# Kernel tuning notes

Measured on AMD Instinct MI355X. Metric: run time of the kernel, lower is better.

The kernel has to match this reference:

```python
import jax, jax.numpy as jnp
import numpy as np

PI = 3.1415926  # matches the truncated pi used in the torch source
BS = 8          # DCT block size (qmat.shape[1:] == (8, 8))
NQ = 16         # number of learned quant matrices (qmat.shape[0])
IMG = 64        # nn.Fold output_size=(64, 64)


def dct_matrix(n):
    # Reproduces the (slightly nonstandard) basis built in DCT2d.__init__.
    C = np.zeros((n, n), dtype=np.float32)
    C[0, :] = np.sqrt(1.0 / n)
    for i in range(1, n):
        for j in range(n):
            C[i, j] = np.cos(PI * i * (2 * j + 1) / (2.0 * n)) * np.sqrt(2.0 / n)
    return jnp.asarray(C)


def setup_inputs() -> dict:
    key = jax.random.key(0)
    ks = jax.random.split(key, 9)
    B, Ch = 32, 256
    x = jax.random.normal(ks[0], (B, Ch, IMG, IMG), dtype=jnp.float32)
    noise_level = jax.random.uniform(ks[1], (1,), dtype=jnp.float32)
    # learned parameters
    qmat = jax.random.uniform(ks[2], (NQ, BS, BS), dtype=jnp.float32)
    qmat_weights = jnp.ones((NQ,), dtype=jnp.float32)
    # noise_level_net: Linear(1,16) -> GELU -> Linear(16,16) -> GELU -> Linear(16, 2+NQ)
    w1 = jax.random.normal(ks[3], (1, 16), dtype=jnp.float32) * 0.5
    b1 = jnp.zeros((16,), dtype=jnp.float32)
    w2 = jax.random.normal(ks[4], (16, 16), dtype=jnp.float32) * 0.25
    b2 = jnp.zeros((16,), dtype=jnp.float32)
    w3 = jax.random.normal(ks[5], (16, 2 + NQ), dtype=jnp.float32) * 0.25
    b3 = jnp.zeros((2 + NQ,), dtype=jnp.float32)
    return {"x": x, "noise_level": noise_level, "qmat": qmat,
            "qmat_weights": qmat_weights, "w1": w1, "b1": b1,
            "w2": w2, "b2": b2, "w3": w3, "b3": b3}


def reference(x, noise_level, qmat, qmat_weights, w1, b1, w2, b2, w3, b3):
    B, Ch, H, W = x.shape
    Cm = dct_matrix(BS)
    Cmt = Cm.T

    # noise_level_net (torch.nn.GELU default = exact erf)
    h = jax.nn.gelu(noise_level @ w1 + b1, approximate=False)
    h = jax.nn.gelu(h @ w2 + b2, approximate=False)
    nr = h @ w3 + b3  # [2 + NQ]

    qw = jax.nn.softmax(qmat_weights) * nr[0] + nr[1]          # [NQ]
    learned_qmat = jnp.einsum('i,ihw->hw', qw * nr[2:], qmat)  # [8, 8]

    # unfold into non-overlapping 8x8 blocks: [B*Ch, L, 8, 8], L = (H/8)*(W/8)
    blocks = x.reshape(B * Ch, H // BS, BS, W // BS, BS)
    blocks = blocks.transpose(0, 1, 3, 2, 4).reshape(B * Ch, -1, BS, BS)

    # 2D DCT per block: C @ X @ C^T
    blocks_dct = jnp.einsum('ij,nljk,km->nlim', Cm, blocks, Cmt)
    # IDCT of mask-weighted spectra: C^T @ X @ C
    low = jnp.einsum('ij,nljk,km->nlim', Cmt, blocks_dct * learned_qmat, Cm)
    high = jnp.einsum('ij,nljk,km->nlim', Cmt, blocks_dct * (1.0 - learned_qmat), Cm)

    def fold(b):  # inverse of the unfold above
        b = b.reshape(B * Ch, H // BS, W // BS, BS, BS)
        return b.transpose(0, 1, 3, 2, 4).reshape(B, Ch, H, W)

    return fold(low), fold(high)
```

## Files before the change

kernel.cpp:

```cpp
#include <hip/hip_runtime.h>
#include <math.h>


typedef float f4 __attribute__((ext_vector_type(4)));

__host__ __device__ constexpr float cc(int i, int j) {
  constexpr double COS16[32] = {
     1.0,
     0.98078528040323043,
     0.92387953251128674,
     0.83146961230254524,
     0.70710678118654752,
     0.55557023301960222,
     0.38268343236508977,
     0.19509032201612827,
     0.0,
    -0.19509032201612827,
    -0.38268343236508977,
    -0.55557023301960222,
    -0.70710678118654752,
    -0.83146961230254524,
    -0.92387953251128674,
    -0.98078528040323043,
    -1.0,
    -0.98078528040323043,
    -0.92387953251128674,
    -0.83146961230254524,
    -0.70710678118654752,
    -0.55557023301960222,
    -0.38268343236508977,
    -0.19509032201612827,
     0.0,
     0.19509032201612827,
     0.38268343236508977,
     0.55557023301960222,
     0.70710678118654752,
     0.83146961230254524,
     0.92387953251128674,
     0.98078528040323043,
  };
  return (i == 0) ? 0.35355339059327373f
                  : (float)(0.5 * COS16[(i * (2 * j + 1)) % 32]);
}

__global__ void setup_q(const float* __restrict__ noise,
                        const float* __restrict__ qmat,
                        const float* __restrict__ qmw,
                        const float* __restrict__ w1, const float* __restrict__ b1,
                        const float* __restrict__ w2, const float* __restrict__ b2,
                        const float* __restrict__ w3, const float* __restrict__ b3,
                        float* __restrict__ qout) {
  __shared__ double coeff[16];
  if (threadIdx.x == 0) {
    const double inv_sqrt2 = 0.70710678118654752;
    double h1[16], h2[16], nr[18];
    double nl = (double)noise[0];
    for (int j = 0; j < 16; ++j) {
      double v = nl * (double)w1[j] + (double)b1[j];
      h1[j] = 0.5 * v * (1.0 + erf(v * inv_sqrt2));
    }
    for (int j = 0; j < 16; ++j) {
      double v = (double)b2[j];
      for (int i = 0; i < 16; ++i) v += h1[i] * (double)w2[i * 16 + j];
      h2[j] = 0.5 * v * (1.0 + erf(v * inv_sqrt2));
    }
    for (int j = 0; j < 18; ++j) {
      double v = (double)b3[j];
      for (int i = 0; i < 16; ++i) v += h2[i] * (double)w3[i * 18 + j];
      nr[j] = v;
    }
    double mx = (double)qmw[0];
    for (int i = 1; i < 16; ++i) mx = fmax(mx, (double)qmw[i]);
    double e[16], s = 0.0;
    for (int i = 0; i < 16; ++i) { e[i] = exp((double)qmw[i] - mx); s += e[i]; }
    for (int i = 0; i < 16; ++i)
      coeff[i] = (e[i] / s * nr[0] + nr[1]) * nr[2 + i];
  }
  __syncthreads();
  const int t = threadIdx.x;
  double q = 0.0;
  for (int i = 0; i < 16; ++i) q += coeff[i] * (double)qmat[i * 64 + t];
  qout[t] = (float)q;
}

__global__ __launch_bounds__(256) void dct_main(const float* __restrict__ x,
                                                const float* __restrict__ qg,
                                                float* __restrict__ lo,
                                                float* __restrict__ hi) {
  __shared__ float Qs[64];
  const int tid = threadIdx.x;
  if (tid < 64) Qs[tid] = qg[tid];
  __syncthreads();

  const int gid = blockIdx.x * 256 + tid;
  const int base = ((gid >> 6) << 12) | (((gid >> 3) & 7) << 9) | ((gid & 7) << 3);
  const float* px = x + base;

  float X[8][8];
#pragma unroll
  for (int r = 0; r < 8; ++r) {
    const f4 a = __builtin_nontemporal_load(reinterpret_cast<const f4*>(px + r * 64));
    const f4 b = __builtin_nontemporal_load(reinterpret_cast<const f4*>(px + r * 64 + 4));
    X[r][0] = a.x; X[r][1] = a.y; X[r][2] = a.z; X[r][3] = a.w;
    X[r][4] = b.x; X[r][5] = b.y; X[r][6] = b.z; X[r][7] = b.w;
  }

  float U[8][8];
#pragma unroll
  for (int r = 0; r < 8; ++r) {
#pragma unroll
    for (int j = 0; j < 8; ++j) {
      float s = X[r][0] * cc(j, 0);
#pragma unroll
      for (int l = 1; l < 8; ++l) s = fmaf(X[r][l], cc(j, l), s);
      U[r][j] = s;
    }
  }
#pragma unroll
  for (int j = 0; j < 8; ++j) {
    float t[8];
#pragma unroll
    for (int i = 0; i < 8; ++i) {
      float s = cc(i, 0) * U[0][j];
#pragma unroll
      for (int k = 1; k < 8; ++k) s = fmaf(cc(i, k), U[k][j], s);
      t[i] = s;
    }
#pragma unroll
    for (int i = 0; i < 8; ++i) U[i][j] = t[i] * Qs[i * 8 + j];
  }
#pragma unroll
  for (int r = 0; r < 8; ++r) {
    float t[8];
#pragma unroll
    for (int j = 0; j < 8; ++j) {
      float s = U[r][0] * cc(0, j);
#pragma unroll
      for (int k = 1; k < 8; ++k) s = fmaf(U[r][k], cc(k, j), s);
      t[j] = s;
    }
#pragma unroll
    for (int j = 0; j < 8; ++j) U[r][j] = t[j];
  }
#pragma unroll
  for (int j = 0; j < 8; ++j) {
    float t[8];
#pragma unroll
    for (int i = 0; i < 8; ++i) {
      float s = cc(0, i) * U[0][j];
#pragma unroll
      for (int k = 1; k < 8; ++k) s = fmaf(cc(k, i), U[k][j], s);
      t[i] = s;
    }
#pragma unroll
    for (int i = 0; i < 8; ++i) U[i][j] = t[i];
  }

  float* plo = lo + base;
  float* phi = hi + base;
#pragma unroll
  for (int r = 0; r < 8; ++r) {
    f4 a = {U[r][0], U[r][1], U[r][2], U[r][3]};
    f4 b = {U[r][4], U[r][5], U[r][6], U[r][7]};
    *reinterpret_cast<f4*>(plo + r * 64)     = a;
    *reinterpret_cast<f4*>(plo + r * 64 + 4) = b;
    f4 c = {X[r][0] - U[r][0], X[r][1] - U[r][1],
            X[r][2] - U[r][2], X[r][3] - U[r][3]};
    f4 d = {X[r][4] - U[r][4], X[r][5] - U[r][5],
            X[r][6] - U[r][6], X[r][7] - U[r][7]};
    *reinterpret_cast<f4*>(phi + r * 64)     = c;
    *reinterpret_cast<f4*>(phi + r * 64 + 4) = d;
  }
}

extern "C" void kernel_launch(void* const* d_in, const int* in_sizes, int n_in,
                              void* d_out, int out_size, void* d_ws, size_t ws_size,
                              hipStream_t stream) {
  const float* x   = (const float*)d_in[0];
  const float* nl  = (const float*)d_in[1];
  const float* qm  = (const float*)d_in[2];
  const float* qmw = (const float*)d_in[3];
  const float* w1  = (const float*)d_in[4];
  const float* b1  = (const float*)d_in[5];
  const float* w2  = (const float*)d_in[6];
  const float* b2  = (const float*)d_in[7];
  const float* w3  = (const float*)d_in[8];
  const float* b3  = (const float*)d_in[9];

  const int n_elem = in_sizes[0];
  float* lo = (float*)d_out;
  float* hi = lo + n_elem;
  float* q  = (float*)d_ws;

  setup_q<<<1, 64, 0, stream>>>(nl, qm, qmw, w1, b1, w2, b2, w3, b3, q);

  const int n_blocks8 = n_elem >> 6;
  const int grid = n_blocks8 >> 8;
  dct_main<<<grid, 256, 0, stream>>>(x, q, lo, hi);
}
```

Baseline: 429.9 us.

## Split each 8x8 DCT block across 8 lanes with shuffle transposes

Instead of one thread holding a whole 8x8 block in registers, each wave now processes 8 blocks with every lane holding one row, and transposes between passes with three xor-shuffle stages. This cuts per-thread register pressure, raising occupancy (launch bounds now request 8 blocks per SM). Each lane's row load is now strided, but lanes in a wave cover contiguous 512-element bands for better coalescing. The trade-off is extra cross-lane shuffle instructions.

```diff
diff --git a/kernel.cpp b/kernel.cpp
--- a/kernel.cpp
+++ b/kernel.cpp
@@ -83,93 +83,95 @@
   qout[t] = (float)q;
 }
 
-__global__ __launch_bounds__(256) void dct_main(const float* __restrict__ x,
-                                                const float* __restrict__ qg,
-                                                float* __restrict__ lo,
-                                                float* __restrict__ hi) {
+__device__ __forceinline__ void transpose8(float v[8], int r) {
+#pragma unroll
+  for (int k = 0; k < 3; ++k) {
+    const int bit = 1 << k;
+    const int lm = 8 << k;
+    const bool rb = (r >> k) & 1;
+#pragma unroll
+    for (int j0 = 0; j0 < 8; ++j0) {
+      if (j0 & bit) continue;
+      const int j1 = j0 | bit;
+      float s = rb ? v[j0] : v[j1];
+      float t = __shfl_xor(s, lm, 64);
+      v[j0] = rb ? t : v[j0];
+      v[j1] = rb ? v[j1] : t;
+    }
+  }
+}
+
+__global__ __launch_bounds__(256, 8) void dct_main(const float* __restrict__ x,
+                                                   const float* __restrict__ qg,
+                                                   float* __restrict__ lo,
+                                                   float* __restrict__ hi) {
   __shared__ float Qs[64];
   const int tid = threadIdx.x;
   if (tid < 64) Qs[tid] = qg[tid];
   __syncthreads();
 
-  const int gid = blockIdx.x * 256 + tid;
-  const int base = ((gid >> 6) << 12) | (((gid >> 3) & 7) << 9) | ((gid & 7) << 3);
-  const float* px = x + base;
-
-  float X[8][8];
-#pragma unroll
-  for (int r = 0; r < 8; ++r) {
-    const f4 a = __builtin_nontemporal_load(reinterpret_cast<const f4*>(px + r * 64));
-    const f4 b = __builtin_nontemporal_load(reinterpret_cast<const f4*>(px + r * 64 + 4));
-    X[r][0] = a.x; X[r][1] = a.y; X[r][2] = a.z; X[r][3] = a.w;
-    X[r][4] = b.x; X[r][5] = b.y; X[r][6] = b.z; X[r][7] = b.w;
-  }
-
-  float U[8][8];
-#pragma unroll
-  for (int r = 0; r < 8; ++r) {
-#pragma unroll
-    for (int j = 0; j < 8; ++j) {
-      float s = X[r][0] * cc(j, 0);
-#pragma unroll
-      for (int l = 1; l < 8; ++l) s = fmaf(X[r][l], cc(j, l), s);
-      U[r][j] = s;
-    }
-  }
-#pragma unroll
-  for (int j = 0; j < 8; ++j) {
-    float t[8];
-#pragma unroll
-    for (int i = 0; i < 8; ++i) {
-      float s = cc(i, 0) * U[0][j];
-#pragma unroll
-      for (int k = 1; k < 8; ++k) s = fmaf(cc(i, k), U[k][j], s);
-      t[i] = s;
-    }
-#pragma unroll
-    for (int i = 0; i < 8; ++i) U[i][j] = t[i] * Qs[i * 8 + j];
-  }
-#pragma unroll
-  for (int r = 0; r < 8; ++r) {
-    float t[8];
-#pragma unroll
-    for (int j = 0; j < 8; ++j) {
-      float s = U[r][0] * cc(0, j);
-#pragma unroll
-      for (int k = 1; k < 8; ++k) s = fmaf(U[r][k], cc(k, j), s);
-      t[j] = s;
-    }
-#pragma unroll
-    for (int j = 0; j < 8; ++j) U[r][j] = t[j];
-  }
-#pragma unroll
-  for (int j = 0; j < 8; ++j) {
-    float t[8];
-#pragma unroll
-    for (int i = 0; i < 8; ++i) {
-      float s = cc(0, i) * U[0][j];
-#pragma unroll
-      for (int k = 1; k < 8; ++k) s = fmaf(cc(k, i), U[k][j], s);
-      t[i] = s;
-    }
-#pragma unroll
-    for (int i = 0; i < 8; ++i) U[i][j] = t[i];
-  }
-
-  float* plo = lo + base;
-  float* phi = hi + base;
-#pragma unroll
-  for (int r = 0; r < 8; ++r) {
-    f4 a = {U[r][0], U[r][1], U[r][2], U[r][3]};
-    f4 b = {U[r][4], U[r][5], U[r][6], U[r][7]};
-    *reinterpret_cast<f4*>(plo + r * 64)     = a;
-    *reinterpret_cast<f4*>(plo + r * 64 + 4) = b;
-    f4 c = {X[r][0] - U[r][0], X[r][1] - U[r][1],
-            X[r][2] - U[r][2], X[r][3] - U[r][3]};
-    f4 d = {X[r][4] - U[r][4], X[r][5] - U[r][5],
-            X[r][6] - U[r][6], X[r][7] - U[r][7]};
-    *reinterpret_cast<f4*>(phi + r * 64)     = c;
-    *reinterpret_cast<f4*>(phi + r * 64 + 4) = d;
+  const int lane = tid & 63;
+  const int r = lane >> 3;
+  const int wave_id = (blockIdx.x * 256 + tid) >> 6;
+  const int base = ((wave_id >> 3) << 12) | ((wave_id & 7) << 9);
+  const int off = base + r * 64 + (lane & 7) * 8;
+
+  float qv[8];
+#pragma unroll
+  for (int j = 0; j < 8; ++j) qv[j] = Qs[j * 8 + r];
+
+  const float* px = x + off;
+  float X[8];
+  {
+    const f4 a = __builtin_nontemporal_load(reinterpret_cast<const f4*>(px));
+    const f4 b = __builtin_nontemporal_load(reinterpret_cast<const f4*>(px + 4));
+    X[0] = a.x; X[1] = a.y; X[2] = a.z; X[3] = a.w;
+    X[4] = b.x; X[5] = b.y; X[6] = b.z; X[7] = b.w;
+  }
+
+  float A[8], B[8];
+#pragma unroll
+  for (int j = 0; j < 8; ++j) {
+    float s = X[0] * cc(j, 0);
+#pragma unroll
+    for (int l = 1; l < 8; ++l) s = fmaf(X[l], cc(j, l), s);
+    A[j] = s;
+  }
+  transpose8(A, r);
+#pragma unroll
+  for (int j = 0; j < 8; ++j) {
+    float s = A[0] * cc(j, 0);
+#pragma unroll
+    for (int l = 1; l < 8; ++l) s = fmaf(A[l], cc(j, l), s);
+    B[j] = s * qv[j];
+  }
+#pragma unroll
+  for (int j = 0; j < 8; ++j) {
+    float s = B[0] * cc(0, j);
+#pragma unroll
+    for (int k = 1; k < 8; ++k) s = fmaf(B[k], cc(k, j), s);
+    A[j] = s;
+  }
+  transpose8(A, r);
+#pragma unroll
+  for (int j = 0; j < 8; ++j) {
+    float s = A[0] * cc(0, j);
+#pragma unroll
+    for (int k = 1; k < 8; ++k) s = fmaf(A[k], cc(k, j), s);
+    B[j] = s;
+  }
+
+  float* plo = lo + off;
+  float* phi = hi + off;
+  {
+    f4 a = {B[0], B[1], B[2], B[3]};
+    f4 b = {B[4], B[5], B[6], B[7]};
+    *reinterpret_cast<f4*>(plo)     = a;
+    *reinterpret_cast<f4*>(plo + 4) = b;
+    f4 c = {X[0] - B[0], X[1] - B[1], X[2] - B[2], X[3] - B[3]};
+    f4 d = {X[4] - B[4], X[5] - B[5], X[6] - B[6], X[7] - B[7]};
+    *reinterpret_cast<f4*>(phi)     = c;
+    *reinterpret_cast<f4*>(phi + 4) = d;
   }
 }
 
@@ -194,7 +196,7 @@
 
   setup_q<<<1, 64, 0, stream>>>(nl, qm, qmw, w1, b1, w2, b2, w3, b3, q);
 
-  const int n_blocks8 = n_elem >> 6;
-  const int grid = n_blocks8 >> 8;
+  const int n_bands = n_elem >> 9;
+  const int grid = (n_bands * 64) / 256;
   dct_main<<<grid, 256, 0, stream>>>(x, q, lo, hi);
 }
```

Result: faster. 419.3 us (-2.4%).
